# Kernel optimization log

Hardware: AMD Instinct MI355X
Metric: run time of the kernel (lower is better)

Reference implementation:

```python
import jax, jax.numpy as jnp
import numpy as np

N_HEADS = 16

def setup_inputs() -> dict:
    key = jax.random.key(0)
    k1, k2, k3 = jax.random.split(key, 3)
    B, L, D = 2, 2048, 1024
    x = jax.random.normal(k1, (B, L, D), dtype=jnp.float32)
    w_qkv = jax.random.normal(k2, (D, 3 * D), dtype=jnp.float32) * (1.0 / np.sqrt(D))
    w_out = jax.random.normal(k3, (D, D), dtype=jnp.float32) * (1.0 / np.sqrt(D))
    return {"x": x, "w_qkv": w_qkv, "w_out": w_out}

def reference(x, w_qkv, w_out):
    B, L, D = x.shape
    H = N_HEADS
    dh = D // H
    qkv = x @ w_qkv                      # (B, L, 3D)
    q, k, v = jnp.split(qkv, 3, axis=-1)
    # (B, H, L, dh)
    q = q.reshape(B, L, H, dh).transpose(0, 2, 1, 3)
    k = k.reshape(B, L, H, dh).transpose(0, 2, 1, 3)
    v = v.reshape(B, L, H, dh).transpose(0, 2, 1, 3)
    scale = 1.0 / jnp.sqrt(jnp.asarray(dh, x.dtype))
    attn = jnp.einsum('bhqd,bhkd->bhqk', q, k) * scale   # (B, H, L, L)
    causal = jnp.tril(jnp.ones((L, L), dtype=bool))
    attn = jnp.where(causal[None, None], attn, -jnp.inf)
    attn = jax.nn.softmax(attn, axis=-1)
    out = jnp.einsum('bhqk,bhkd->bhqd', attn, v)         # (B, H, L, dh)
    out = out.transpose(0, 2, 1, 3).reshape(B, L, D)
    return out @ w_out
```

## Files before the change

kernel.cpp:

```cpp
#include <hip/hip_runtime.h>

typedef __attribute__((ext_vector_type(4))) float f32x4;
typedef __attribute__((ext_vector_type(16))) float f32x16;
typedef __attribute__((ext_vector_type(8))) __bf16 bf16x8;
typedef __attribute__((ext_vector_type(4))) __bf16 bf16x4;
typedef __attribute__((ext_vector_type(4))) unsigned u32x4;
typedef __attribute__((ext_vector_type(2))) unsigned u32x2;

static __device__ __forceinline__ f32x4 mfma16(bf16x8 a, bf16x8 b, f32x4 c) {
    return __builtin_amdgcn_mfma_f32_16x16x32_bf16(a, b, c, 0, 0, 0);
}
static __device__ __forceinline__ f32x16 mfma32(bf16x8 a, bf16x8 b, f32x16 c) {
    return __builtin_amdgcn_mfma_f32_32x32x16_bf16(a, b, c, 0, 0, 0);
}
static __device__ __forceinline__ unsigned pk_bf16(float a, float b) {
    unsigned lo = __builtin_bit_cast(unsigned short, (__bf16)a);
    unsigned hh = __builtin_bit_cast(unsigned short, (__bf16)b);
    return lo | (hh << 16);
}

#define QSCALE 0.18033688f

__global__ __launch_bounds__(256) void prep_all(const float* __restrict__ x,
                                                __bf16* __restrict__ xb,
                                                const float* __restrict__ wq,
                                                __bf16* __restrict__ wqT,
                                                const float* __restrict__ wo,
                                                __bf16* __restrict__ woT) {
    __shared__ float t[32][33];
    int bid = blockIdx.x, tid = threadIdx.x;
    if (bid < 4096) {
        int i = bid * 256 + tid;
        f32x4 v = ((const f32x4*)x)[i];
        bf16x4 o;
#pragma unroll
        for (int j = 0; j < 4; j++) o[j] = (__bf16)v[j];
        ((bf16x4*)xb)[i] = o;
        return;
    }
    const float* in;
    __bf16* out;
    int R, C, bx, by;
    if (bid < 4096 + 3072) {
        int b2 = bid - 4096;
        in = wq; out = wqT; R = 1024; C = 3072;
        bx = (b2 % 96) * 32; by = (b2 / 96) * 32;
    } else {
        int b2 = bid - 7168;
        in = wo; out = woT; R = 1024; C = 1024;
        bx = (b2 % 32) * 32; by = (b2 / 32) * 32;
    }
    int tx = tid & 31, ty = tid >> 5;
#pragma unroll
    for (int k = 0; k < 32; k += 8)
        t[ty + k][tx] = in[(size_t)(by + ty + k) * C + bx + tx];
    __syncthreads();
#pragma unroll
    for (int k = 0; k < 32; k += 8)
        out[(size_t)(bx + ty + k) * R + by + tx] = (__bf16)t[tx][ty + k];
}

#define BM 128
#define BN 128
#define BKG 64

template <int MODE>
__global__ __launch_bounds__(256) void gemm_bt(const __bf16* __restrict__ A,
                                               const __bf16* __restrict__ Bt,
                                               int M, int N, int K,
                                               float* __restrict__ Cout,
                                               __bf16* __restrict__ Qf,
                                               __bf16* __restrict__ Kf,
                                               __bf16* __restrict__ Vf) {
    __shared__ __attribute__((aligned(16))) __bf16 As[BM * BKG];
    __shared__ __attribute__((aligned(16))) __bf16 Bs[BN * BKG];
    int tid = threadIdx.x;
    int wave = tid >> 6, lane = tid & 63;
    int lrow = lane & 15, lgrp = lane >> 4;
    int chunk = gridDim.x >> 3;
    int bid = blockIdx.x;
    int swz = (bid & 7) * chunk + (bid >> 3);
    int nbx = N >> 7;
    int m0 = (swz / nbx) * BM, n0 = (swz % nbx) * BN;
    int wm = (wave >> 1) * 64, wn = (wave & 1) * 64;

    f32x4 acc[4][4];
#pragma unroll
    for (int i = 0; i < 4; i++)
#pragma unroll
        for (int j = 0; j < 4; j++) acc[i][j] = (f32x4){0.f, 0.f, 0.f, 0.f};

    int srow = tid >> 3;
    int gch = (tid & 7) ^ (srow & 7);
    const __bf16* aSrc = A + (size_t)(m0 + srow) * K + gch * 8;
    const __bf16* bSrc = Bt + (size_t)(n0 + srow) * K + gch * 8;

    for (int k0 = 0; k0 < K; k0 += BKG) {
#pragma unroll
        for (int c = 0; c < 4; c++) {
            __builtin_amdgcn_global_load_lds(
                (const __attribute__((address_space(1))) void*)(aSrc + k0 + (size_t)c * 32 * K),
                (__attribute__((address_space(3))) void*)(As + (c * 256 + wave * 64) * 8),
                16, 0, 0);
        }
#pragma unroll
        for (int c = 0; c < 4; c++) {
            __builtin_amdgcn_global_load_lds(
                (const __attribute__((address_space(1))) void*)(bSrc + k0 + (size_t)c * 32 * K),
                (__attribute__((address_space(3))) void*)(Bs + (c * 256 + wave * 64) * 8),
                16, 0, 0);
        }
        __syncthreads();
#pragma unroll
        for (int kk = 0; kk < 2; kk++) {
            bf16x8 af[4], bfr[4];
#pragma unroll
            for (int mt = 0; mt < 4; mt++) {
                int row = wm + mt * 16 + lrow;
                int slot = row * 8 + ((4 * kk + lgrp) ^ (row & 7));
                af[mt] = *(const bf16x8*)(As + slot * 8);
            }
#pragma unroll
            for (int nt = 0; nt < 4; nt++) {
                int row = wn + nt * 16 + lrow;
                int slot = row * 8 + ((4 * kk + lgrp) ^ (row & 7));
                bfr[nt] = *(const bf16x8*)(Bs + slot * 8);
            }
#pragma unroll
            for (int mt = 0; mt < 4; mt++)
#pragma unroll
                for (int nt = 0; nt < 4; nt++)
                    acc[mt][nt] = mfma16(af[mt], bfr[nt], acc[mt][nt]);
        }
        __syncthreads();
    }

#pragma unroll
    for (int mt = 0; mt < 4; mt++) {
#pragma unroll
        for (int nt = 0; nt < 4; nt++) {
            int f0 = m0 + wm + mt * 16 + lgrp * 4;
            int t = n0 + wn + nt * 16 + lrow;
            if (MODE == 0) {
                *(f32x4*)(Cout + (size_t)t * M + f0) = acc[mt][nt];
            } else {
                int which = f0 >> 10, hn = f0 & 1023;
                int h = hn >> 6, d0 = hn & 63;
                int b = t >> 11, li = t & 2047;
                int bh = b * 16 + h, c = li >> 5, tl = li & 31;
                size_t bhbase = (size_t)bh * 131072;
                if (which == 2) {
                    int ks = tl >> 4, hv = (tl >> 3) & 1, jv = tl & 7;
                    size_t base =
                        bhbase + ((size_t)(c * 4 + ks * 2 + hv) * 64 + d0) * 8 + jv;
#pragma unroll
                    for (int r = 0; r < 4; r++)
                        Vf[base + (size_t)r * 8] = (__bf16)acc[mt][nt][r];
                } else {
                    int st = d0 >> 4, hv = (d0 >> 3) & 1, j0 = d0 & 7;
                    size_t idx =
                        bhbase + ((size_t)(c * 8 + st * 2 + hv) * 32 + tl) * 8 + j0;
                    bf16x4 pv;
                    if (which == 0) {
#pragma unroll
                        for (int r = 0; r < 4; r++)
                            pv[r] = (__bf16)(acc[mt][nt][r] * QSCALE);
                        *(bf16x4*)(Qf + idx) = pv;
                    } else {
#pragma unroll
                        for (int r = 0; r < 4; r++) pv[r] = (__bf16)acc[mt][nt][r];
                        *(bf16x4*)(Kf + idx) = pv;
                    }
                }
            }
        }
    }
}

template <bool MASKED>
static __device__ __forceinline__ void attn_chunk(
    int c, int ql, int hi, const __bf16* __restrict__ Kp,
    const __bf16* __restrict__ Vp, const bf16x8 (&qf)[4], bf16x8 ones,
    f32x16& o0, f32x16& o1, f32x16& lsa) {
    const __bf16* kb = Kp + ((size_t)c * 8 + hi) * 256 + ql * 8;
    bf16x8 kf[4];
#pragma unroll
    for (int st = 0; st < 4; st++) kf[st] = *(const bf16x8*)(kb + st * 512);
    const __bf16* vb = Vp + ((size_t)c * 4 + hi) * 512 + ql * 8;
    bf16x8 v00 = *(const bf16x8*)(vb);
    bf16x8 v01 = *(const bf16x8*)(vb + 256);
    bf16x8 v10 = *(const bf16x8*)(vb + 1024);
    bf16x8 v11 = *(const bf16x8*)(vb + 1280);

    f32x16 sa;
#pragma unroll
    for (int r = 0; r < 16; r++) sa[r] = 0.f;
#pragma unroll
    for (int st = 0; st < 4; st++) sa = mfma32(kf[st], qf[st], sa);

    float p[16];
#pragma unroll
    for (int r = 0; r < 16; r++) {
        float s = sa[r];
        if (MASKED) {
            int krel = (r & 3) + 8 * (r >> 2) + 4 * hi;
            if (krel > ql) s = -1e30f;
        }
        p[r] = __builtin_amdgcn_exp2f(s);
    }

    unsigned w[8];
#pragma unroll
    for (int i = 0; i < 8; i++) w[i] = pk_bf16(p[2 * i], p[2 * i + 1]);
    u32x2 r02 = __builtin_amdgcn_permlane32_swap(w[0], w[2], false, false);
    u32x2 r13 = __builtin_amdgcn_permlane32_swap(w[1], w[3], false, false);
    u32x2 r46 = __builtin_amdgcn_permlane32_swap(w[4], w[6], false, false);
    u32x2 r57 = __builtin_amdgcn_permlane32_swap(w[5], w[7], false, false);
    bf16x8 pa0 = __builtin_bit_cast(bf16x8, (u32x4){r02[0], r13[0], r02[1], r13[1]});
    bf16x8 pa1 = __builtin_bit_cast(bf16x8, (u32x4){r46[0], r57[0], r46[1], r57[1]});

    o0 = mfma32(pa0, v00, o0);
    o1 = mfma32(pa0, v01, o1);
    lsa = mfma32(pa0, ones, lsa);
    o0 = mfma32(pa1, v10, o0);
    o1 = mfma32(pa1, v11, o1);
    lsa = mfma32(pa1, ones, lsa);
}

__global__ __launch_bounds__(256, 4) void attn_fwd10(const __bf16* __restrict__ Qf,
                                                     const __bf16* __restrict__ Kf,
                                                     const __bf16* __restrict__ Vf,
                                                     __bf16* __restrict__ Ob) {
    __shared__ float comb[3][64][49];
    int tid = threadIdx.x;
    int wave = tid >> 6, lane = tid & 63;
    int ql = lane & 31, hi = lane >> 5;
    int bid = blockIdx.x;
    int xcd = bid & 7, idx = bid >> 3;
    int bh = xcd * 4 + (idx >> 6);
    int strip = 63 - (idx & 63);
    int q0 = strip * 32;

    const __bf16* Qp = Qf + (size_t)bh * 131072;
    const __bf16* Kp = Kf + (size_t)bh * 131072;
    const __bf16* Vp = Vf + (size_t)bh * 131072;

    const __bf16* qb = Qp + ((size_t)strip * 8 + hi) * 256 + ql * 8;
    bf16x8 qf[4];
#pragma unroll
    for (int st = 0; st < 4; st++) qf[st] = *(const bf16x8*)(qb + st * 512);

    bf16x8 ones;
#pragma unroll
    for (int j = 0; j < 8; j++) ones[j] = (__bf16)1.0f;

    f32x16 o0, o1, lsa;
#pragma unroll
    for (int r = 0; r < 16; r++) { o0[r] = 0.f; o1[r] = 0.f; lsa[r] = 0.f; }

    for (int c = wave; c < strip; c += 4)
        attn_chunk<false>(c, ql, hi, Kp, Vp, qf, ones, o0, o1, lsa);
    if ((strip & 3) == wave)
        attn_chunk<true>(strip, ql, hi, Kp, Vp, qf, ones, o0, o1, lsa);

    if (wave >= 1) {
        float* sl = &comb[wave - 1][lane][0];
#pragma unroll
        for (int r = 0; r < 16; r++) {
            sl[r] = o0[r]; sl[16 + r] = o1[r]; sl[32 + r] = lsa[r];
        }
    }
    __syncthreads();
    if (wave == 0) {
#pragma unroll
        for (int s = 0; s < 3; s++) {
            const float* sl = &comb[s][lane][0];
#pragma unroll
            for (int r = 0; r < 16; r++) {
                o0[r] += sl[r]; o1[r] += sl[16 + r]; lsa[r] += sl[32 + r];
            }
        }
        int b = bh >> 4, h = bh & 15;
#pragma unroll
        for (int r = 0; r < 16; r++) {
            int crow = (r & 3) + 8 * (r >> 2) + 4 * hi;
            float inv;
            asm("v_rcp_f32 %0, %1" : "=v"(inv) : "v"(lsa[r]));
            size_t base = ((size_t)(b * 2048 + q0 + crow)) * 1024 + h * 64;
            Ob[base + ql] = (__bf16)(o0[r] * inv);
            Ob[base + 32 + ql] = (__bf16)(o1[r] * inv);
        }
    }
}

extern "C" void kernel_launch(void* const* d_in, const int* in_sizes, int n_in,
                              void* d_out, int out_size, void* d_ws, size_t ws_size,
                              hipStream_t stream) {
    const float* x = (const float*)d_in[0];
    const float* w_qkv = (const float*)d_in[1];
    const float* w_out = (const float*)d_in[2];
    float* out = (float*)d_out;

    char* ws = (char*)d_ws;
    __bf16* xb    = (__bf16*)(ws);
    __bf16* wqkvT = (__bf16*)(ws + (size_t)(8  << 20));
    __bf16* woutT = (__bf16*)(ws + (size_t)(14 << 20));
    __bf16* Qf    = (__bf16*)(ws + (size_t)(16 << 20));
    __bf16* Kf    = (__bf16*)(ws + (size_t)(24 << 20));
    __bf16* Vf    = (__bf16*)(ws + (size_t)(32 << 20));
    __bf16* Ob    = (__bf16*)(ws + (size_t)(40 << 20));

    prep_all<<<8192, 256, 0, stream>>>(x, xb, w_qkv, wqkvT, w_out, woutT);
    gemm_bt<1><<<768, 256, 0, stream>>>(
        wqkvT, xb, 3072, 4096, 1024, nullptr, Qf, Kf, Vf);
    attn_fwd10<<<2048, 256, 0, stream>>>(Qf, Kf, Vf, Ob);
    gemm_bt<0><<<256, 256, 0, stream>>>(
        woutT, Ob, 1024, 4096, 1024, out, nullptr, nullptr, nullptr);
}
```

Baseline: 103.4 us.

## Template GEMM M-tile, shrink output projection tile, remap QKV block order

Makes the GEMM M-tile size a template parameter and runs the output projection with 64-row tiles on 512 blocks instead of 128-row tiles on 256 blocks, so more workgroups fill the 256 CUs. It also replaces the QKV GEMM's swizzle with an explicit mapping that gives each group of 8 consecutive blocks a distinct region, spreading them across XCDs for L2 locality. Smaller tiles lower per-block arithmetic intensity and add operand reloads from memory.

```diff
diff --git a/kernel.cpp b/kernel.cpp
--- a/kernel.cpp
+++ b/kernel.cpp
@@ -60,11 +60,10 @@
         out[(size_t)(bx + ty + k) * R + by + tx] = (__bf16)t[tx][ty + k];
 }
 
-#define BM 128
 #define BN 128
 #define BKG 64
 
-template <int MODE>
+template <int MODE, int BMv>
 __global__ __launch_bounds__(256) void gemm_bt(const __bf16* __restrict__ A,
                                                const __bf16* __restrict__ Bt,
                                                int M, int N, int K,
@@ -72,21 +71,33 @@
                                                __bf16* __restrict__ Qf,
                                                __bf16* __restrict__ Kf,
                                                __bf16* __restrict__ Vf) {
-    __shared__ __attribute__((aligned(16))) __bf16 As[BM * BKG];
+    constexpr int nMt = BMv / 32;
+    __shared__ __attribute__((aligned(16))) __bf16 As[BMv * BKG];
     __shared__ __attribute__((aligned(16))) __bf16 Bs[BN * BKG];
     int tid = threadIdx.x;
     int wave = tid >> 6, lane = tid & 63;
     int lrow = lane & 15, lgrp = lane >> 4;
-    int chunk = gridDim.x >> 3;
     int bid = blockIdx.x;
-    int swz = (bid & 7) * chunk + (bid >> 3);
-    int nbx = N >> 7;
-    int m0 = (swz / nbx) * BM, n0 = (swz % nbx) * BN;
-    int wm = (wave >> 1) * 64, wn = (wave & 1) * 64;
-
-    f32x4 acc[4][4];
-#pragma unroll
-    for (int i = 0; i < 4; i++)
+    int m0, n0;
+    if (MODE == 1) {
+        int x = bid & 7, j = bid >> 3;
+        int mx = x & 1, nx = x >> 1;
+        int mi = j >> 3, ni = j & 7;
+        m0 = (mx * 12 + mi) * BMv;
+        n0 = (nx * 8 + ni) * BN;
+    } else {
+        int chunk = gridDim.x >> 3;
+        int swz = (bid & 7) * chunk + (bid >> 3);
+        int nbx = N >> 7;
+        m0 = (swz / nbx) * BMv;
+        n0 = (swz % nbx) * BN;
+    }
+    int wm = (wave >> 1) * (BMv / 2);
+    int wn = (wave & 1) * 64;
+
+    f32x4 acc[nMt][4];
+#pragma unroll
+    for (int i = 0; i < nMt; i++)
 #pragma unroll
         for (int j = 0; j < 4; j++) acc[i][j] = (f32x4){0.f, 0.f, 0.f, 0.f};
 
@@ -97,7 +108,7 @@
 
     for (int k0 = 0; k0 < K; k0 += BKG) {
 #pragma unroll
-        for (int c = 0; c < 4; c++) {
+        for (int c = 0; c < BMv / 32; c++) {
             __builtin_amdgcn_global_load_lds(
                 (const __attribute__((address_space(1))) void*)(aSrc + k0 + (size_t)c * 32 * K),
                 (__attribute__((address_space(3))) void*)(As + (c * 256 + wave * 64) * 8),
@@ -113,9 +124,9 @@
         __syncthreads();
 #pragma unroll
         for (int kk = 0; kk < 2; kk++) {
-            bf16x8 af[4], bfr[4];
-#pragma unroll
-            for (int mt = 0; mt < 4; mt++) {
+            bf16x8 af[nMt], bfr[4];
+#pragma unroll
+            for (int mt = 0; mt < nMt; mt++) {
                 int row = wm + mt * 16 + lrow;
                 int slot = row * 8 + ((4 * kk + lgrp) ^ (row & 7));
                 af[mt] = *(const bf16x8*)(As + slot * 8);
@@ -127,7 +138,7 @@
                 bfr[nt] = *(const bf16x8*)(Bs + slot * 8);
             }
 #pragma unroll
-            for (int mt = 0; mt < 4; mt++)
+            for (int mt = 0; mt < nMt; mt++)
 #pragma unroll
                 for (int nt = 0; nt < 4; nt++)
                     acc[mt][nt] = mfma16(af[mt], bfr[nt], acc[mt][nt]);
@@ -136,7 +147,7 @@
     }
 
 #pragma unroll
-    for (int mt = 0; mt < 4; mt++) {
+    for (int mt = 0; mt < nMt; mt++) {
 #pragma unroll
         for (int nt = 0; nt < 4; nt++) {
             int f0 = m0 + wm + mt * 16 + lgrp * 4;
@@ -311,9 +322,9 @@
     __bf16* Ob    = (__bf16*)(ws + (size_t)(40 << 20));
 
     prep_all<<<8192, 256, 0, stream>>>(x, xb, w_qkv, wqkvT, w_out, woutT);
-    gemm_bt<1><<<768, 256, 0, stream>>>(
+    gemm_bt<1, 128><<<768, 256, 0, stream>>>(
         wqkvT, xb, 3072, 4096, 1024, nullptr, Qf, Kf, Vf);
     attn_fwd10<<<2048, 256, 0, stream>>>(Qf, Kf, Vf, Ob);
-    gemm_bt<0><<<256, 256, 0, stream>>>(
+    gemm_bt<0, 64><<<512, 256, 0, stream>>>(
         woutT, Ob, 1024, 4096, 1024, out, nullptr, nullptr, nullptr);
 }
```

Measured after the change: 97.13 us. 6.1% less time.
